# Performance work log

Hardware: AMD Instinct MI355X
Metric: run time of the kernel (lower is better)

## Reference

```python
import jax, jax.numpy as jnp
import numpy as np

N, F_IN, H, OUT, L = 100000, 32, 128, 200, 4
E = 1600000
EPS = 1e-5


def setup_inputs() -> dict:
    key = jax.random.key(0)
    ks = jax.random.split(key, 16)
    glorot = lambda k, shape: jax.random.uniform(k, shape, jnp.float32, -1.0, 1.0) * jnp.sqrt(6.0 / (shape[0] + shape[1]))
    return {
        'x': jax.random.normal(ks[0], (N, F_IN), jnp.float32),
        'edge_index': jax.random.randint(ks[1], (2, E), 0, N, jnp.int32),
        'W_emb': glorot(ks[2], (F_IN, H)), 'b_emb': jnp.zeros((H,), jnp.float32),
        'W_conv': jnp.stack([glorot(jax.random.fold_in(ks[3], i), (H, H)) for i in range(L)]),
        'b_conv': jnp.zeros((L, H), jnp.float32),
        'ln_g': jnp.ones((L, H), jnp.float32), 'ln_b': jnp.zeros((L, H), jnp.float32),
        'W_res': jnp.stack([glorot(jax.random.fold_in(ks[4], i), (H, H)) for i in range(L // 2)]),
        'b_res': jnp.zeros((L // 2, H), jnp.float32),
        'W_fc1': glorot(ks[5], (H, H)), 'b_fc1': jnp.zeros((H,), jnp.float32),
        'fcn_g': jnp.ones((H,), jnp.float32), 'fcn_b': jnp.zeros((H,), jnp.float32),
        'W_fc2': glorot(ks[6], (H, OUT)), 'b_fc2': jnp.zeros((OUT,), jnp.float32),
    }


def _layer_norm(h, g, b):
    mu = jnp.mean(h, axis=-1, keepdims=True)
    var = jnp.mean(jnp.square(h - mu), axis=-1, keepdims=True)
    return (h - mu) * jax.lax.rsqrt(var + EPS) * g + b


def reference(x, edge_index, W_emb, b_emb, W_conv, b_conv, ln_g, ln_b,
              W_res, b_res, W_fc1, b_fc1, fcn_g, fcn_b, W_fc2, b_fc2):
    n = x.shape[0]
    # GCN normalization with self-loops (computed once; same every layer)
    self_idx = jnp.arange(n, dtype=edge_index.dtype)
    src = jnp.concatenate([edge_index[0], self_idx])
    dst = jnp.concatenate([edge_index[1], self_idx])
    deg = jax.ops.segment_sum(jnp.ones_like(src, jnp.float32), dst, num_segments=n)
    dinv = jnp.where(deg > 0, jax.lax.rsqrt(jnp.maximum(deg, 1.0)), 0.0)
    norm = dinv[src] * dinv[dst]  # [E+N]

    h = x @ W_emb + b_emb  # node embedding [N, H]
    for i in range(L):
        residual = (h @ W_res[i // 2 - 1] + b_res[i // 2 - 1]) if (i % 2 == 0 and i > 0) else h
        # GCNConv: transform, gather by src, scale, scatter-add to dst
        ht = h @ W_conv[i]
        msg = norm[:, None] * ht[src]
        h = jax.ops.segment_sum(msg, dst, num_segments=n) + b_conv[i]
        h = jax.nn.relu(_layer_norm(h, ln_g[i], ln_b[i]))
        h = h + residual  # shapes always match ([N, H])
    # no batch vector -> global mean pool over all nodes
    h = jnp.mean(h, axis=0, keepdims=True)  # [1, H]
    h = jax.nn.relu(_layer_norm(h @ W_fc1 + b_fc1, fcn_g, fcn_b))
    return h @ W_fc2 + b_fc2  # [1, OUT]
```

## Files before the change

kernel.cpp:

```cpp
#include <hip/hip_runtime.h>

constexpr int N_NODES = 100000;
constexpr int F_IN    = 32;
constexpr int H       = 128;
constexpr int OUT_F   = 200;
constexpr int NEDGES  = 1600000;
constexpr float EPS   = 1e-5f;

constexpr int WS_BLKS    = 80;
constexpr int TILE_BLKS  = (N_NODES + 63) / 64;
constexpr int MM_BLKS    = TILE_BLKS * 2;
constexpr int AGG_BLKS   = N_NODES / 32;

constexpr int NB     = (N_NODES + 127) / 128;
constexpr int BCAP   = 2560;
constexpr int P1_EPT = 16, P1_THR = 512;
constexpr int P1_EPB = P1_THR * P1_EPT;
constexpr int P1_BLKS = (NEDGES + P1_EPB - 1) / P1_EPB;
constexpr int P2_IT  = BCAP / 256;
constexpr int WQ_BLKS = NEDGES / 4 / 256;

typedef __attribute__((ext_vector_type(8))) short  short8;
typedef __attribute__((ext_vector_type(4))) float  f32x4;
typedef __attribute__((ext_vector_type(2))) float  fv2;

__device__ __forceinline__ void fma4(float4& a, float s, const float4& w) {
  a.x = fmaf(s, w.x, a.x); a.y = fmaf(s, w.y, a.y);
  a.z = fmaf(s, w.z, a.z); a.w = fmaf(s, w.w, a.w);
}

__device__ __forceinline__ unsigned short f2bf(float f) {
  union { float f; unsigned u; } v; v.f = f;
  unsigned r = v.u + 0x7fffu + ((v.u >> 16) & 1u);
  return (unsigned short)(r >> 16);
}
__device__ __forceinline__ float bflo(unsigned u) { return __uint_as_float(u << 16); }
__device__ __forceinline__ float bfhi(unsigned u) { return __uint_as_float(u & 0xffff0000u); }
__device__ __forceinline__ unsigned pack2(float lo, float hi) {
  return (unsigned)f2bf(lo) | ((unsigned)f2bf(hi) << 16);
}
__device__ __forceinline__ void st_bf4(unsigned short* p, float4 v) {
  uint2 o; o.x = pack2(v.x, v.y); o.y = pack2(v.z, v.w);
  *(uint2*)p = o;
}

#if __has_builtin(__builtin_amdgcn_cvt_pk_f32_fp8) && __has_builtin(__builtin_amdgcn_cvt_pk_fp8_f32)
#define HAVE_FP8_CVT 1
#endif

#ifndef HAVE_FP8_CVT
__device__ __forceinline__ float fp8_dec1(unsigned b) {
  unsigned s = (b >> 7) & 1u, E = (b >> 3) & 15u, m = b & 7u;
  float v;
  if (E) {
    union { unsigned u; float f; } t;
    t.u = (s << 31) | ((E + 120u) << 23) | (m << 20);
    v = t.f;
  } else {
    v = (s ? -1.f : 1.f) * (float)m * 0.001953125f;
  }
  return v;
}
#endif

template <bool HI>
__device__ __forceinline__ fv2 fp8x2(unsigned u) {
#ifdef HAVE_FP8_CVT
  return __builtin_amdgcn_cvt_pk_f32_fp8((int)u, HI);
#else
  unsigned p = HI ? (u >> 16) : u;
  fv2 r; r.x = fp8_dec1(p & 0xffu); r.y = fp8_dec1((p >> 8) & 0xffu);
  return r;
#endif
}

__device__ __forceinline__ unsigned char f32_to_fp8(float f) {
#ifdef HAVE_FP8_CVT
  return (unsigned char)(__builtin_amdgcn_cvt_pk_fp8_f32(f, f, 0, false) & 0xff);
#else
  union { float f; unsigned u; } t; t.f = f;
  unsigned s = t.u >> 31;
  float a = fabsf(f);
  if (a > 448.f) a = 448.f;
  t.f = a;
  int e = (int)((t.u >> 23) & 0xff) - 127;
  unsigned char r;
  if (a == 0.f) {
    r = 0;
  } else if (e >= -6) {
    unsigned m = t.u & 0x7fffffu;
    unsigned keep = m >> 20, rest = m & 0xfffffu;
    keep += (rest > 0x80000u) || (rest == 0x80000u && (keep & 1u));
    int E = e + 7;
    if (keep == 8u) { keep = 0u; E += 1; }
    if (E >= 16) { E = 15; keep = 6u; }
    r = (unsigned char)((E << 3) | keep);
  } else {
    int mi = (int)(a * 512.f + 0.5f);
    r = (mi > 7) ? (unsigned char)(1u << 3) : (unsigned char)mi;
  }
  return (unsigned char)(r | (s << 7));
#endif
}

__global__ void k_ws(const float* __restrict__ W_conv,
                     const float* __restrict__ W_res,
                     unsigned short* __restrict__ whiT) {
  int base = blockIdx.x * 1024;
#pragma unroll
  for (int j = 0; j < 4; ++j) {
    int idx = base + j * 256 + threadIdx.x;
    if (idx < 5 * H * H) {
      int m = idx >> 14, rr = idx & 16383;
      int k = rr >> 7, n = rr & 127;
      const float* src = (m < 4) ? (W_conv + m * H * H) : W_res;
      whiT[m * H * H + n * H + k] = f2bf(src[k * H + n]);
    }
  }
}

__device__ __forceinline__ void mm_lds_fp8(const unsigned short* sA,
                                           const unsigned short* __restrict__ WT,
                                           int n0, int t,
                                           unsigned char* __restrict__ htOut) {
  int wave = t >> 6, lane = t & 63;
  int wr = wave >> 1, wc = wave & 1;
  int m = lane & 15, quad = (lane >> 4) & 3;
  short8 bh[4][4];
#pragma unroll
  for (int q = 0; q < 4; ++q)
#pragma unroll
    for (int ct = 0; ct < 4; ++ct) {
      int n = wc * 64 + ct * 16 + m;
      bh[q][ct] = *(const short8*)(WT + n * H + q * 32 + quad * 8);
    }
  f32x4 acc[2][4];
#pragma unroll
  for (int i = 0; i < 2; ++i)
#pragma unroll
    for (int j = 0; j < 4; ++j) acc[i][j] = (f32x4){0.f, 0.f, 0.f, 0.f};
#pragma unroll
  for (int q = 0; q < 4; ++q) {
    short8 ah[2];
#pragma unroll
    for (int rt = 0; rt < 2; ++rt)
      ah[rt] = *(const short8*)(sA + (wr * 32 + rt * 16 + m) * 136 + q * 32 + quad * 8);
#pragma unroll
    for (int rt = 0; rt < 2; ++rt)
#pragma unroll
      for (int ct = 0; ct < 4; ++ct)
        acc[rt][ct] = __builtin_amdgcn_mfma_f32_16x16x32_bf16(ah[rt], bh[q][ct], acc[rt][ct], 0, 0, 0);
  }
#pragma unroll
  for (int rt = 0; rt < 2; ++rt)
#pragma unroll
    for (int ct = 0; ct < 4; ++ct) {
      int col = wc * 64 + ct * 16 + m;
#pragma unroll
      for (int rr = 0; rr < 4; ++rr) {
        int gn = n0 + wr * 32 + rt * 16 + quad * 4 + rr;
        if (gn < N_NODES) htOut[(size_t)gn * H + col] = f32_to_fp8(acc[rt][ct][rr]);
      }
    }
}

__global__ __launch_bounds__(256) void k_embed(
    const float* __restrict__ x, const float* __restrict__ W_emb,
    const float* __restrict__ b_emb, unsigned short* __restrict__ h,
    const unsigned short* __restrict__ W0T, unsigned char* __restrict__ ht8) {
  __shared__ __align__(16) char smem[25600];
  int t = threadIdx.x;
  int n0 = blockIdx.x * 64;
  float* sW = (float*)smem;
  float* sX = sW + 4096;
  unsigned short* sH = (unsigned short*)smem;
#pragma unroll
  for (int p = 0; p < 4; ++p)
    ((float4*)sW)[t + p * 256] = ((const float4*)W_emb)[t + p * 256];
#pragma unroll
  for (int p = 0; p < 2; ++p) {
    int fi = t * 2 + p;
    int row = fi >> 3, k4 = (fi & 7) * 4;
    int gn = n0 + row; if (gn >= N_NODES) gn = N_NODES - 1;
    *(float4*)(sX + row * 36 + k4) = *(const float4*)(x + (size_t)gn * F_IN + k4);
  }
  __syncthreads();
  int nr = t >> 2, col0 = (t & 3) * 4;
  float4 acc[8];
#pragma unroll
  for (int i = 0; i < 8; ++i) acc[i] = make_float4(0.f, 0.f, 0.f, 0.f);
#pragma unroll 4
  for (int k = 0; k < F_IN; ++k) {
    float xv = sX[nr * 36 + k];
    const float* wp = sW + k * H + col0;
#pragma unroll
    for (int i = 0; i < 8; ++i) fma4(acc[i], xv, *(const float4*)(wp + i * 16));
  }
#pragma unroll
  for (int i = 0; i < 8; ++i) {
    float4 bv = *(const float4*)(b_emb + col0 + i * 16);
    acc[i].x += bv.x; acc[i].y += bv.y; acc[i].z += bv.z; acc[i].w += bv.w;
  }
  __syncthreads();
  int node = n0 + nr;
  unsigned short* hr = h + (size_t)node * H + col0;
#pragma unroll
  for (int i = 0; i < 8; ++i) {
    st_bf4(sH + nr * 136 + col0 + i * 16, acc[i]);
    if (node < N_NODES) st_bf4(hr + i * 16, acc[i]);
  }
  __syncthreads();
  mm_lds_fp8(sH, W0T, n0, t, ht8);
}

__global__ __launch_bounds__(512) void k_p1(const int* __restrict__ ei,
                                            int* __restrict__ bcnt,
                                            unsigned* __restrict__ bscr) {
  __shared__ int hist[NB];
  __shared__ int hbase[NB];
  int t = threadIdx.x;
  for (int i = t; i < NB; i += 512) hist[i] = 0;
  __syncthreads();
  int e0 = blockIdx.x * P1_EPB;
  unsigned pk[P1_EPT]; int br[P1_EPT];
#pragma unroll
  for (int k = 0; k < P1_EPT; ++k) {
    int e = e0 + k * 512 + t;
    if (e < NEDGES) {
      int src = ei[e];
      int dst = ei[NEDGES + e];
      int b = dst >> 7;
      pk[k] = ((unsigned)src << 7) | (unsigned)(dst & 127);
      int r = atomicAdd(&hist[b], 1);
      br[k] = (b << 13) | r;
    } else {
      br[k] = -1; pk[k] = 0;
    }
  }
  __syncthreads();
  for (int i = t; i < NB; i += 512) {
    int c = hist[i];
    hbase[i] = c ? atomicAdd(&bcnt[i], c) : 0;
  }
  __syncthreads();
#pragma unroll
  for (int k = 0; k < P1_EPT; ++k) {
    if (br[k] >= 0) {
      int b = br[k] >> 13, r = br[k] & 8191;
      int pos = hbase[b] + r;
      if (pos < BCAP) bscr[(size_t)b * BCAP + pos] = pk[k];
    }
  }
}

__global__ void k_scanbc(const int* __restrict__ bcnt, int* __restrict__ bbase) {
  __shared__ int s[1024];
  int t = threadIdx.x;
  int d = (t < NB) ? bcnt[t] : 0;
  s[t] = d;
  __syncthreads();
#pragma unroll
  for (int off = 1; off < 1024; off <<= 1) {
    int v = (t >= off) ? s[t - off] : 0;
    __syncthreads();
    s[t] += v;
    __syncthreads();
  }
  if (t < NB) bbase[t] = s[t] - d;
}

__global__ __launch_bounds__(256) void k_p2(const unsigned* __restrict__ bscr,
                                            const int* __restrict__ bcnt,
                                            const int* __restrict__ bbase,
                                            int* __restrict__ degT,
                                            int* __restrict__ offs,
                                            float* __restrict__ dinv,
                                            unsigned* __restrict__ csr) {
  __shared__ int dl[128], sc[128];
  int b = blockIdx.x, t = threadIdx.x;
  if (t < 128) dl[t] = 0;
  __syncthreads();
  int n = min(bcnt[b], BCAP);
  int base = bbase[b];
  const unsigned* seg = bscr + (size_t)b * BCAP;
  unsigned pk[P2_IT]; unsigned short rr[P2_IT];
#pragma unroll
  for (int k = 0; k < P2_IT; ++k) {
    int i = k * 256 + t;
    if (i < n) {
      unsigned p = seg[i];
      pk[k] = p;
      rr[k] = (unsigned short)atomicAdd(&dl[p & 127u], 1);
    } else pk[k] = 0xffffffffu;
  }
  __syncthreads();
  if (t < 128) sc[t] = dl[t];
  __syncthreads();
#pragma unroll
  for (int off = 1; off < 128; off <<= 1) {
    int v = (t >= off && t < 128) ? sc[t - off] : 0;
    __syncthreads();
    if (t < 128) sc[t] += v;
    __syncthreads();
  }
  if (t < 128) {
    int node = b * 128 + t;
    if (node < N_NODES) {
      int d = dl[t];
      degT[node] = d;
      dinv[node] = rsqrtf((float)(d + 1));
      offs[node] = base + sc[t] - d;
    }
  }
  __syncthreads();
#pragma unroll
  for (int k = 0; k < P2_IT; ++k) {
    if (pk[k] != 0xffffffffu) {
      unsigned p = pk[k];
      unsigned dlo = p & 127u;
      int pos = base + (sc[dlo] - dl[dlo]) + (int)rr[k];
      csr[pos] = (p >> 7) << 15;
    }
  }
}

__global__ __launch_bounds__(256) void k_wq(unsigned* __restrict__ csr,
                                            const float* __restrict__ dinv) {
  int i = (blockIdx.x * 256 + threadIdx.x) * 4;
  if (i < NEDGES) {
    uint4 e = *(uint4*)(csr + i);
    e.x |= (unsigned)(dinv[e.x >> 15] * 32767.f + 0.5f);
    e.y |= (unsigned)(dinv[e.y >> 15] * 32767.f + 0.5f);
    e.z |= (unsigned)(dinv[e.z >> 15] * 32767.f + 0.5f);
    e.w |= (unsigned)(dinv[e.w >> 15] * 32767.f + 0.5f);
    *(uint4*)(csr + i) = e;
  }
}

struct MMAcc { f32x4 a[2][2]; };

__device__ __forceinline__ MMAcc mm_core(const unsigned short* __restrict__ A,
                                         const unsigned short* __restrict__ WhiT,
                                         int n0, int c0, int t,
                                         unsigned short* sA) {
  int wave = t >> 6, lane = t & 63;
  int wr = wave >> 1, wc = wave & 1;
  int m = lane & 15, quad = (lane >> 4) & 3;
  short8 bh[4][2];
#pragma unroll
  for (int q = 0; q < 4; ++q)
#pragma unroll
    for (int ct = 0; ct < 2; ++ct) {
      int n = c0 + wc * 32 + ct * 16 + m;
      bh[q][ct] = *(const short8*)(WhiT + n * H + q * 32 + quad * 8);
    }
#pragma unroll
  for (int p = 0; p < 4; ++p) {
    int fi = t + p * 256;
    int row = fi >> 4, c8 = (fi & 15) * 8;
    int gn = n0 + row; if (gn >= N_NODES) gn = N_NODES - 1;
    *(uint4*)(sA + row * 136 + c8) = *(const uint4*)(A + (size_t)gn * H + c8);
  }
  __syncthreads();
  MMAcc r;
#pragma unroll
  for (int i = 0; i < 2; ++i)
#pragma unroll
    for (int j = 0; j < 2; ++j) r.a[i][j] = (f32x4){0.f, 0.f, 0.f, 0.f};
#pragma unroll
  for (int q = 0; q < 4; ++q) {
    short8 ah[2];
#pragma unroll
    for (int rt = 0; rt < 2; ++rt)
      ah[rt] = *(const short8*)(sA + (wr * 32 + rt * 16 + m) * 136 + q * 32 + quad * 8);
#pragma unroll
    for (int rt = 0; rt < 2; ++rt)
#pragma unroll
      for (int ct = 0; ct < 2; ++ct)
        r.a[rt][ct] = __builtin_amdgcn_mfma_f32_16x16x32_bf16(ah[rt], bh[q][ct], r.a[rt][ct], 0, 0, 0);
  }
  return r;
}

__device__ __forceinline__ void mm_store_fp8(const MMAcc& r, unsigned char* ht8,
                                             int n0, int c0, int t) {
  int wave = t >> 6, lane = t & 63;
  int wr = wave >> 1, wc = wave & 1;
  int m = lane & 15, quad = (lane >> 4) & 3;
#pragma unroll
  for (int rt = 0; rt < 2; ++rt)
#pragma unroll
    for (int ct = 0; ct < 2; ++ct) {
      int col = c0 + wc * 32 + ct * 16 + m;
#pragma unroll
      for (int rr = 0; rr < 4; ++rr) {
        int gn = n0 + wr * 32 + rt * 16 + quad * 4 + rr;
        if (gn < N_NODES) ht8[(size_t)gn * H + col] = f32_to_fp8(r.a[rt][ct][rr]);
      }
    }
}

__global__ __launch_bounds__(256) void k_mm(const unsigned short* __restrict__ A,
                                            const unsigned short* __restrict__ WhiT,
                                            unsigned char* __restrict__ ht8) {
  __shared__ __align__(16) unsigned short sA[64 * 136];
  int j = blockIdx.x;
  int n0 = (j >> 1) * 64, c0 = (j & 1) * 64;
  MMAcc r = mm_core(A, WhiT, n0, c0, threadIdx.x, sA);
  mm_store_fp8(r, ht8, n0, c0, threadIdx.x);
}

__global__ __launch_bounds__(256) void k_mmd(const unsigned short* __restrict__ A,
    const unsigned short* __restrict__ WcT, const unsigned short* __restrict__ WrT,
    const float* __restrict__ bias,
    unsigned char* __restrict__ ht8, unsigned short* __restrict__ resb) {
  __shared__ __align__(16) unsigned short sA[64 * 136];
  int t = threadIdx.x;
  int j = blockIdx.x;
  int n0 = (j >> 1) * 64, c0 = (j & 1) * 64;
  int wave = t >> 6, lane = t & 63;
  int wr = wave >> 1, wc = wave & 1;
  int m = lane & 15, quad = (lane >> 4) & 3;
  short8 bhc[4][2], bhr[4][2];
#pragma unroll
  for (int q = 0; q < 4; ++q)
#pragma unroll
    for (int ct = 0; ct < 2; ++ct) {
      int n = c0 + wc * 32 + ct * 16 + m;
      bhc[q][ct] = *(const short8*)(WcT + n * H + q * 32 + quad * 8);
      bhr[q][ct] = *(const short8*)(WrT + n * H + q * 32 + quad * 8);
    }
#pragma unroll
  for (int p = 0; p < 4; ++p) {
    int fi = t + p * 256;
    int row = fi >> 4, c8 = (fi & 15) * 8;
    int gn = n0 + row; if (gn >= N_NODES) gn = N_NODES - 1;
    *(uint4*)(sA + row * 136 + c8) = *(const uint4*)(A + (size_t)gn * H + c8);
  }
  __syncthreads();
  f32x4 accC[2][2], accR[2][2];
#pragma unroll
  for (int i = 0; i < 2; ++i)
#pragma unroll
    for (int jj = 0; jj < 2; ++jj) {
      accC[i][jj] = (f32x4){0.f, 0.f, 0.f, 0.f};
      accR[i][jj] = (f32x4){0.f, 0.f, 0.f, 0.f};
    }
#pragma unroll
  for (int q = 0; q < 4; ++q) {
    short8 ah[2];
#pragma unroll
    for (int rt = 0; rt < 2; ++rt)
      ah[rt] = *(const short8*)(sA + (wr * 32 + rt * 16 + m) * 136 + q * 32 + quad * 8);
#pragma unroll
    for (int rt = 0; rt < 2; ++rt)
#pragma unroll
      for (int ct = 0; ct < 2; ++ct) {
        accC[rt][ct] = __builtin_amdgcn_mfma_f32_16x16x32_bf16(ah[rt], bhc[q][ct], accC[rt][ct], 0, 0, 0);
        accR[rt][ct] = __builtin_amdgcn_mfma_f32_16x16x32_bf16(ah[rt], bhr[q][ct], accR[rt][ct], 0, 0, 0);
      }
  }
#pragma unroll
  for (int rt = 0; rt < 2; ++rt)
#pragma unroll
    for (int ct = 0; ct < 2; ++ct) {
      int col = c0 + wc * 32 + ct * 16 + m;
      float bv = bias[col];
#pragma unroll
      for (int rr = 0; rr < 4; ++rr) {
        int gn = n0 + wr * 32 + rt * 16 + quad * 4 + rr;
        if (gn < N_NODES) {
          ht8[(size_t)gn * H + col]  = f32_to_fp8(accC[rt][ct][rr]);
          resb[(size_t)gn * H + col] = f2bf(accR[rt][ct][rr] + bv);
        }
      }
    }
}

__device__ __forceinline__ void agg_round8(const unsigned char* __restrict__ ht8,
                                           unsigned flo, int gbase, int e0,
                                           int s, float w, fv2* acc2) {
  uint2 uu[8]; float ww[8];
#pragma unroll
  for (int jj = 0; jj < 8; ++jj) {
    int ss = __shfl(s, gbase + e0 + jj, 64);
    ww[jj] = __shfl(w, gbase + e0 + jj, 64);
    uu[jj] = *(const uint2*)(ht8 + (((unsigned)ss << 7) | flo));
  }
#pragma unroll
  for (int jj = 0; jj < 8; ++jj) {
    float we = ww[jj];
    fv2 we2 = {we, we};
    acc2[0] += we2 * fp8x2<false>(uu[jj].x);
    acc2[1] += we2 * fp8x2<true>(uu[jj].x);
    acc2[2] += we2 * fp8x2<false>(uu[jj].y);
    acc2[3] += we2 * fp8x2<true>(uu[jj].y);
  }
}

__global__ __launch_bounds__(512) void k_agg(
    const unsigned char* __restrict__ ht8, const unsigned short* __restrict__ res,
    const float* __restrict__ dinv, const int* __restrict__ offs,
    const int* __restrict__ degT, const unsigned* __restrict__ csr,
    const float* __restrict__ bias, const float* __restrict__ lng,
    const float* __restrict__ lnb, unsigned short* __restrict__ hout) {
  int t = threadIdx.x;
  int fl = t & 15;
  int gbase = t & 48;
  int node = blockIdx.x * 32 + (t >> 4);
  unsigned flo = (unsigned)fl * 8u;
  int start = offs[node], cnt = degT[node];
  float di = dinv[node];
  fv2 acc2[4];
  {
    uint2 u = *(const uint2*)(ht8 + (((unsigned)node << 7) | flo));
    float sw = di * di;
    fv2 sw2 = {sw, sw};
    acc2[0] = sw2 * fp8x2<false>(u.x);
    acc2[1] = sw2 * fp8x2<true>(u.x);
    acc2[2] = sw2 * fp8x2<false>(u.y);
    acc2[3] = sw2 * fp8x2<true>(u.y);
  }
  float ddq = di * (1.f / 32767.f);
  for (int b0 = 0; b0 < cnt; b0 += 16) {
    int m = min(16, cnt - b0);
    int s = node; float w = 0.f;
    if (fl < m) {
      unsigned ev = csr[start + b0 + fl];
      s = (int)(ev >> 15);
      w = (float)(ev & 32767u) * ddq;
    }
    agg_round8(ht8, flo, gbase, 0, s, w, acc2);
    if (m > 8) agg_round8(ht8, flo, gbase, 8, s, w, acc2);
  }
  float acc[8] = {acc2[0].x, acc2[0].y, acc2[1].x, acc2[1].y,
                  acc2[2].x, acc2[2].y, acc2[3].x, acc2[3].y};
  float4 b0v = *(const float4*)(bias + fl * 8);
  float4 b1v = *(const float4*)(bias + fl * 8 + 4);
  acc[0] += b0v.x; acc[1] += b0v.y; acc[2] += b0v.z; acc[3] += b0v.w;
  acc[4] += b1v.x; acc[5] += b1v.y; acc[6] += b1v.z; acc[7] += b1v.w;
  float sl = ((acc[0] + acc[1]) + (acc[2] + acc[3])) +
             ((acc[4] + acc[5]) + (acc[6] + acc[7]));
#pragma unroll
  for (int mk = 1; mk <= 8; mk <<= 1) sl += __shfl_xor(sl, mk, 16);
  float mu = sl * (1.f / 128.f);
  float d[8];
  float vl = 0.f;
#pragma unroll
  for (int j = 0; j < 8; ++j) { d[j] = acc[j] - mu; vl = fmaf(d[j], d[j], vl); }
#pragma unroll
  for (int mk = 1; mk <= 8; mk <<= 1) vl += __shfl_xor(vl, mk, 16);
  float rs = rsqrtf(vl * (1.f / 128.f) + EPS);
  float4 g0 = *(const float4*)(lng + fl * 8);
  float4 g1 = *(const float4*)(lng + fl * 8 + 4);
  float4 be0 = *(const float4*)(lnb + fl * 8);
  float4 be1 = *(const float4*)(lnb + fl * 8 + 4);
  uint4 rv = *(const uint4*)(res + (size_t)node * 128 + fl * 8);
  float o0 = fmaxf(fmaf(d[0] * rs, g0.x, be0.x), 0.f) + bflo(rv.x);
  float o1 = fmaxf(fmaf(d[1] * rs, g0.y, be0.y), 0.f) + bfhi(rv.x);
  float o2 = fmaxf(fmaf(d[2] * rs, g0.z, be0.z), 0.f) + bflo(rv.y);
  float o3 = fmaxf(fmaf(d[3] * rs, g0.w, be0.w), 0.f) + bfhi(rv.y);
  float o4 = fmaxf(fmaf(d[4] * rs, g1.x, be1.x), 0.f) + bflo(rv.z);
  float o5 = fmaxf(fmaf(d[5] * rs, g1.y, be1.y), 0.f) + bfhi(rv.z);
  float o6 = fmaxf(fmaf(d[6] * rs, g1.z, be1.z), 0.f) + bflo(rv.w);
  float o7 = fmaxf(fmaf(d[7] * rs, g1.w, be1.w), 0.f) + bfhi(rv.w);
  uint4 ov;
  ov.x = pack2(o0, o1); ov.y = pack2(o2, o3);
  ov.z = pack2(o4, o5); ov.w = pack2(o6, o7);
  *(uint4*)(hout + (size_t)node * 128 + fl * 8) = ov;
}

__global__ __launch_bounds__(256) void k_pool(const unsigned short* __restrict__ h,
                                              float* __restrict__ pool) {
  __shared__ float colsum[128];
  int t = threadIdx.x;
  if (t < 128) colsum[t] = 0.f;
  __syncthreads();
  int lr = t >> 4, seg = t & 15;
  float acc[8] = {0.f, 0.f, 0.f, 0.f, 0.f, 0.f, 0.f, 0.f};
  for (int n = blockIdx.x * 16 + lr; n < N_NODES; n += gridDim.x * 16) {
    uint4 u = *(const uint4*)(h + (size_t)n * H + seg * 8);
    acc[0] += bflo(u.x); acc[1] += bfhi(u.x);
    acc[2] += bflo(u.y); acc[3] += bfhi(u.y);
    acc[4] += bflo(u.z); acc[5] += bfhi(u.z);
    acc[6] += bflo(u.w); acc[7] += bfhi(u.w);
  }
#pragma unroll
  for (int j = 0; j < 8; ++j) atomicAdd(&colsum[seg * 8 + j], acc[j]);
  __syncthreads();
  if (t < 128) atomicAdd(&pool[t], colsum[t]);
}

__global__ void k_head(const float* __restrict__ pool, const float* __restrict__ Wfc1,
                       const float* __restrict__ bfc1, const float* __restrict__ g,
                       const float* __restrict__ bb, const float* __restrict__ Wfc2,
                       const float* __restrict__ bfc2, float* __restrict__ out) {
  __shared__ float sm[128], s1[128], stats[2];
  int t = threadIdx.x;
  if (t < 128) sm[t] = pool[t] * (1.f / (float)N_NODES);
  __syncthreads();
  if (t < 128) {
    float a = bfc1[t];
    for (int k = 0; k < 128; ++k) a = fmaf(sm[k], Wfc1[k * 128 + t], a);
    s1[t] = a;
  }
  __syncthreads();
  if (t == 0) {
    float mu = 0.f;
    for (int k = 0; k < 128; ++k) mu += s1[k];
    mu *= (1.f / 128.f);
    float var = 0.f;
    for (int k = 0; k < 128; ++k) { float d = s1[k] - mu; var += d * d; }
    var *= (1.f / 128.f);
    stats[0] = mu; stats[1] = rsqrtf(var + EPS);
  }
  __syncthreads();
  if (t < 128) s1[t] = fmaxf((s1[t] - stats[0]) * stats[1] * g[t] + bb[t], 0.f);
  __syncthreads();
  if (t < OUT_F) {
    float a = bfc2[t];
    for (int k = 0; k < 128; ++k) a = fmaf(s1[k], Wfc2[k * OUT_F + t], a);
    out[t] = a;
  }
}

extern "C" void kernel_launch(void* const* d_in, const int* in_sizes, int n_in,
                              void* d_out, int out_size, void* d_ws, size_t ws_size,
                              hipStream_t stream) {
  const float* x      = (const float*)d_in[0];
  const int*   ei     = (const int*)d_in[1];
  const float* W_emb  = (const float*)d_in[2];
  const float* b_emb  = (const float*)d_in[3];
  const float* W_conv = (const float*)d_in[4];
  const float* b_conv = (const float*)d_in[5];
  const float* ln_g   = (const float*)d_in[6];
  const float* ln_b   = (const float*)d_in[7];
  const float* W_res  = (const float*)d_in[8];
  const float* b_res  = (const float*)d_in[9];
  const float* W_fc1  = (const float*)d_in[10];
  const float* b_fc1  = (const float*)d_in[11];
  const float* fcn_g  = (const float*)d_in[12];
  const float* fcn_b  = (const float*)d_in[13];
  const float* W_fc2  = (const float*)d_in[14];
  const float* b_fc2  = (const float*)d_in[15];
  float* out = (float*)d_out;

  char* p = (char*)d_ws;
  auto take = [&](size_t bytes) {
    char* r = p; p += (bytes + 255) & ~(size_t)255; return r;
  };
  unsigned short* bufA = (unsigned short*)take((size_t)N_NODES * H * 2);
  unsigned short* bufB = (unsigned short*)take((size_t)N_NODES * H * 2);
  unsigned short* bufC = (unsigned short*)take((size_t)N_NODES * H * 2);
  unsigned char*  ht8  = (unsigned char*)take((size_t)N_NODES * H);
  unsigned short* whiT = (unsigned short*)take((size_t)5 * H * H * 2);
  int*   degT = (int*)take(N_NODES * 4);
  int*   offs = (int*)take(N_NODES * 4);
  float* dinv = (float*)take(N_NODES * 4);
  int*   bcnt = (int*)take(NB * 4);
  int*   bbase= (int*)take(NB * 4);
  unsigned* bscr = (unsigned*)take((size_t)NB * BCAP * 4);
  unsigned* csr  = (unsigned*)take((size_t)NEDGES * 4);
  float* pool = (float*)take(128 * 4);

  (void)hipMemsetAsync(bcnt, 0, NB * 4, stream);
  (void)hipMemsetAsync(pool, 0, 128 * 4, stream);

  k_ws<<<WS_BLKS, 256, 0, stream>>>(W_conv, W_res, whiT);
  k_p1<<<P1_BLKS, P1_THR, 0, stream>>>(ei, bcnt, bscr);
  k_scanbc<<<1, 1024, 0, stream>>>(bcnt, bbase);
  k_p2<<<NB, 256, 0, stream>>>(bscr, bcnt, bbase, degT, offs, dinv, csr);
  k_wq<<<WQ_BLKS, 256, 0, stream>>>(csr, dinv);
  k_embed<<<TILE_BLKS, 256, 0, stream>>>(x, W_emb, b_emb, bufA,
                                         whiT + 0 * H * H, ht8);

  k_agg<<<AGG_BLKS, 512, 0, stream>>>(ht8, bufA, dinv, offs, degT, csr,
                                      b_conv + 0 * H, ln_g + 0 * H, ln_b + 0 * H, bufC);
  k_mm<<<MM_BLKS, 256, 0, stream>>>(bufC, whiT + 1 * H * H, ht8);
  k_agg<<<AGG_BLKS, 512, 0, stream>>>(ht8, bufC, dinv, offs, degT, csr,
                                      b_conv + 1 * H, ln_g + 1 * H, ln_b + 1 * H, bufA);
  k_mmd<<<MM_BLKS, 256, 0, stream>>>(bufA, whiT + 2 * H * H, whiT + 4 * H * H,
                                     b_res, ht8, bufB);
  k_agg<<<AGG_BLKS, 512, 0, stream>>>(ht8, bufB, dinv, offs, degT, csr,
                                      b_conv + 2 * H, ln_g + 2 * H, ln_b + 2 * H, bufC);
  k_mm<<<MM_BLKS, 256, 0, stream>>>(bufC, whiT + 3 * H * H, ht8);
  k_agg<<<AGG_BLKS, 512, 0, stream>>>(ht8, bufC, dinv, offs, degT, csr,
                                      b_conv + 3 * H, ln_g + 3 * H, ln_b + 3 * H, bufA);

  k_pool<<<256, 256, 0, stream>>>(bufA, pool);
  k_head<<<1, 256, 0, stream>>>(pool, W_fc1, b_fc1, fcn_g, fcn_b,
                                W_fc2, b_fc2, out);
}
```

Before: 445.7 us.

## Fold weight conversion into edge binning kernel, widen mm tiles, unify agg rounds

```diff
diff --git a/kernel.cpp b/kernel.cpp
--- a/kernel.cpp
+++ b/kernel.cpp
@@ -7,9 +7,9 @@
 constexpr int NEDGES  = 1600000;
 constexpr float EPS   = 1e-5f;
 
-constexpr int WS_BLKS    = 80;
 constexpr int TILE_BLKS  = (N_NODES + 63) / 64;
-constexpr int MM_BLKS    = TILE_BLKS * 2;
+constexpr int MM_BLKS    = TILE_BLKS;
+constexpr int MMD_BLKS   = TILE_BLKS * 2;
 constexpr int AGG_BLKS   = N_NODES / 32;
 
 constexpr int NB     = (N_NODES + 127) / 128;
@@ -17,6 +17,7 @@
 constexpr int P1_EPT = 16, P1_THR = 512;
 constexpr int P1_EPB = P1_THR * P1_EPT;
 constexpr int P1_BLKS = (NEDGES + P1_EPB - 1) / P1_EPB;
+constexpr int WS_BLKS = 40;
 constexpr int P2_IT  = BCAP / 256;
 constexpr int WQ_BLKS = NEDGES / 4 / 256;
 
@@ -103,22 +104,6 @@
 #endif
 }
 
-__global__ void k_ws(const float* __restrict__ W_conv,
-                     const float* __restrict__ W_res,
-                     unsigned short* __restrict__ whiT) {
-  int base = blockIdx.x * 1024;
-#pragma unroll
-  for (int j = 0; j < 4; ++j) {
-    int idx = base + j * 256 + threadIdx.x;
-    if (idx < 5 * H * H) {
-      int m = idx >> 14, rr = idx & 16383;
-      int k = rr >> 7, n = rr & 127;
-      const float* src = (m < 4) ? (W_conv + m * H * H) : W_res;
-      whiT[m * H * H + n * H + k] = f2bf(src[k * H + n]);
-    }
-  }
-}
-
 __device__ __forceinline__ void mm_lds_fp8(const unsigned short* sA,
                                            const unsigned short* __restrict__ WT,
                                            int n0, int t,
@@ -215,10 +200,25 @@
 
 __global__ __launch_bounds__(512) void k_p1(const int* __restrict__ ei,
                                             int* __restrict__ bcnt,
-                                            unsigned* __restrict__ bscr) {
+                                            unsigned* __restrict__ bscr,
+                                            const float* __restrict__ W_conv,
+                                            const float* __restrict__ W_res,
+                                            unsigned short* __restrict__ whiT) {
   __shared__ int hist[NB];
   __shared__ int hbase[NB];
   int t = threadIdx.x;
+  if (blockIdx.x >= P1_BLKS) {
+    int base = (blockIdx.x - P1_BLKS) * 2048;
+#pragma unroll
+    for (int j = 0; j < 4; ++j) {
+      int idx = base + j * 512 + t;
+      int m = idx >> 14, rr = idx & 16383;
+      int k = rr >> 7, n = rr & 127;
+      const float* src = (m < 4) ? (W_conv + m * H * H) : W_res;
+      whiT[m * H * H + n * H + k] = f2bf(src[k * H + n]);
+    }
+    return;
+  }
   for (int i = t; i < NB; i += 512) hist[i] = 0;
   __syncthreads();
   int e0 = blockIdx.x * P1_EPB;
@@ -337,23 +337,12 @@
   }
 }
 
-struct MMAcc { f32x4 a[2][2]; };
-
-__device__ __forceinline__ MMAcc mm_core(const unsigned short* __restrict__ A,
-                                         const unsigned short* __restrict__ WhiT,
-                                         int n0, int c0, int t,
-                                         unsigned short* sA) {
-  int wave = t >> 6, lane = t & 63;
-  int wr = wave >> 1, wc = wave & 1;
-  int m = lane & 15, quad = (lane >> 4) & 3;
-  short8 bh[4][2];
-#pragma unroll
-  for (int q = 0; q < 4; ++q)
-#pragma unroll
-    for (int ct = 0; ct < 2; ++ct) {
-      int n = c0 + wc * 32 + ct * 16 + m;
-      bh[q][ct] = *(const short8*)(WhiT + n * H + q * 32 + quad * 8);
-    }
+__global__ __launch_bounds__(256) void k_mm(const unsigned short* __restrict__ A,
+                                            const unsigned short* __restrict__ WhiT,
+                                            unsigned char* __restrict__ ht8) {
+  __shared__ __align__(16) unsigned short sA[64 * 136];
+  int t = threadIdx.x;
+  int n0 = blockIdx.x * 64;
 #pragma unroll
   for (int p = 0; p < 4; ++p) {
     int fi = t + p * 256;
@@ -362,52 +351,7 @@
     *(uint4*)(sA + row * 136 + c8) = *(const uint4*)(A + (size_t)gn * H + c8);
   }
   __syncthreads();
-  MMAcc r;
-#pragma unroll
-  for (int i = 0; i < 2; ++i)
-#pragma unroll
-    for (int j = 0; j < 2; ++j) r.a[i][j] = (f32x4){0.f, 0.f, 0.f, 0.f};
-#pragma unroll
-  for (int q = 0; q < 4; ++q) {
-    short8 ah[2];
-#pragma unroll
-    for (int rt = 0; rt < 2; ++rt)
-      ah[rt] = *(const short8*)(sA + (wr * 32 + rt * 16 + m) * 136 + q * 32 + quad * 8);
-#pragma unroll
-    for (int rt = 0; rt < 2; ++rt)
-#pragma unroll
-      for (int ct = 0; ct < 2; ++ct)
-        r.a[rt][ct] = __builtin_amdgcn_mfma_f32_16x16x32_bf16(ah[rt], bh[q][ct], r.a[rt][ct], 0, 0, 0);
-  }
-  return r;
-}
-
-__device__ __forceinline__ void mm_store_fp8(const MMAcc& r, unsigned char* ht8,
-                                             int n0, int c0, int t) {
-  int wave = t >> 6, lane = t & 63;
-  int wr = wave >> 1, wc = wave & 1;
-  int m = lane & 15, quad = (lane >> 4) & 3;
-#pragma unroll
-  for (int rt = 0; rt < 2; ++rt)
-#pragma unroll
-    for (int ct = 0; ct < 2; ++ct) {
-      int col = c0 + wc * 32 + ct * 16 + m;
-#pragma unroll
-      for (int rr = 0; rr < 4; ++rr) {
-        int gn = n0 + wr * 32 + rt * 16 + quad * 4 + rr;
-        if (gn < N_NODES) ht8[(size_t)gn * H + col] = f32_to_fp8(r.a[rt][ct][rr]);
-      }
-    }
-}
-
-__global__ __launch_bounds__(256) void k_mm(const unsigned short* __restrict__ A,
-                                            const unsigned short* __restrict__ WhiT,
-                                            unsigned char* __restrict__ ht8) {
-  __shared__ __align__(16) unsigned short sA[64 * 136];
-  int j = blockIdx.x;
-  int n0 = (j >> 1) * 64, c0 = (j & 1) * 64;
-  MMAcc r = mm_core(A, WhiT, n0, c0, threadIdx.x, sA);
-  mm_store_fp8(r, ht8, n0, c0, threadIdx.x);
+  mm_lds_fp8(sA, WhiT, n0, t, ht8);
 }
 
 __global__ __launch_bounds__(256) void k_mmd(const unsigned short* __restrict__ A,
@@ -477,18 +421,18 @@
     }
 }
 
-__device__ __forceinline__ void agg_round8(const unsigned char* __restrict__ ht8,
-                                           unsigned flo, int gbase, int e0,
-                                           int s, float w, fv2* acc2) {
-  uint2 uu[8]; float ww[8];
-#pragma unroll
-  for (int jj = 0; jj < 8; ++jj) {
-    int ss = __shfl(s, gbase + e0 + jj, 64);
-    ww[jj] = __shfl(w, gbase + e0 + jj, 64);
+__device__ __forceinline__ void agg_round16(const unsigned char* __restrict__ ht8,
+                                            unsigned flo, int gbase,
+                                            int s, float w, fv2* acc2) {
+  uint2 uu[16]; float ww[16];
+#pragma unroll
+  for (int jj = 0; jj < 16; ++jj) {
+    int ss = __shfl(s, gbase + jj, 64);
+    ww[jj] = __shfl(w, gbase + jj, 64);
     uu[jj] = *(const uint2*)(ht8 + (((unsigned)ss << 7) | flo));
   }
 #pragma unroll
-  for (int jj = 0; jj < 8; ++jj) {
+  for (int jj = 0; jj < 16; ++jj) {
     float we = ww[jj];
     fv2 we2 = {we, we};
     acc2[0] += we2 * fp8x2<false>(uu[jj].x);
@@ -523,15 +467,13 @@
   }
   float ddq = di * (1.f / 32767.f);
   for (int b0 = 0; b0 < cnt; b0 += 16) {
-    int m = min(16, cnt - b0);
     int s = node; float w = 0.f;
-    if (fl < m) {
+    if (b0 + fl < cnt) {
       unsigned ev = csr[start + b0 + fl];
       s = (int)(ev >> 15);
       w = (float)(ev & 32767u) * ddq;
     }
-    agg_round8(ht8, flo, gbase, 0, s, w, acc2);
-    if (m > 8) agg_round8(ht8, flo, gbase, 8, s, w, acc2);
+    agg_round16(ht8, flo, gbase, s, w, acc2);
   }
   float acc[8] = {acc2[0].x, acc2[0].y, acc2[1].x, acc2[1].y,
                   acc2[2].x, acc2[2].y, acc2[3].x, acc2[3].y};
@@ -666,8 +608,8 @@
   (void)hipMemsetAsync(bcnt, 0, NB * 4, stream);
   (void)hipMemsetAsync(pool, 0, 128 * 4, stream);
 
-  k_ws<<<WS_BLKS, 256, 0, stream>>>(W_conv, W_res, whiT);
-  k_p1<<<P1_BLKS, P1_THR, 0, stream>>>(ei, bcnt, bscr);
+  k_p1<<<P1_BLKS + WS_BLKS, P1_THR, 0, stream>>>(ei, bcnt, bscr,
+                                                 W_conv, W_res, whiT);
   k_scanbc<<<1, 1024, 0, stream>>>(bcnt, bbase);
   k_p2<<<NB, 256, 0, stream>>>(bscr, bcnt, bbase, degT, offs, dinv, csr);
   k_wq<<<WQ_BLKS, 256, 0, stream>>>(csr, dinv);
@@ -679,8 +621,8 @@
   k_mm<<<MM_BLKS, 256, 0, stream>>>(bufC, whiT + 1 * H * H, ht8);
   k_agg<<<AGG_BLKS, 512, 0, stream>>>(ht8, bufC, dinv, offs, degT, csr,
                                       b_conv + 1 * H, ln_g + 1 * H, ln_b + 1 * H, bufA);
-  k_mmd<<<MM_BLKS, 256, 0, stream>>>(bufA, whiT + 2 * H * H, whiT + 4 * H * H,
-                                     b_res, ht8, bufB);
+  k_mmd<<<MMD_BLKS, 256, 0, stream>>>(bufA, whiT + 2 * H * H, whiT + 4 * H * H,
+                                      b_res, ht8, bufB);
   k_agg<<<AGG_BLKS, 512, 0, stream>>>(ht8, bufB, dinv, offs, degT, csr,
                                       b_conv + 2 * H, ln_g + 2 * H, ln_b + 2 * H, bufC);
   k_mm<<<MM_BLKS, 256, 0, stream>>>(bufC, whiT + 3 * H * H, ht8);
```

Result: faster. 435.5 us, median of 2 (-2.3%).
